# Kernel optimization log

Hardware: AMD Instinct MI355X
Metric: run time of the kernel (lower is better)

The kernel has to match this reference:

```python
import jax, jax.numpy as jnp
import numpy as np

ALPHA = 1.702
LIMIT = 7.0
BLOCK = 32  # mxfp4 block size (values per scale)

# fp4 e2m1 lookup table, indexed by 4-bit code (sign in high bit)
FP4_LUT = jnp.array([0.0, 0.5, 1.0, 1.5, 2.0, 3.0, 4.0, 6.0,
                     -0.0, -0.5, -1.0, -1.5, -2.0, -3.0, -4.0, -6.0],
                    dtype=jnp.float32)


def dequant_mxfp4(blocks, scales):
    # blocks: [E, R, C//2] int byte values (two fp4 nibbles per byte, low nibble first)
    # scales: [E, R, C//32] e8m0 exponents; value = 2^(scale - 127)
    E, R, _ = blocks.shape
    nb = scales.shape[-1]
    lo = blocks & 0xF
    hi = (blocks >> 4) & 0xF
    vals = jnp.stack([FP4_LUT[lo], FP4_LUT[hi]], axis=-1)  # [E,R,C//2,2]
    vals = vals.reshape(E, R, nb, BLOCK)
    scale = jnp.exp2((scales - 127).astype(jnp.float32))   # [E,R,nb]
    return (vals * scale[..., None]).reshape(E, R, nb * BLOCK)  # [E,R,C]


def setup_inputs() -> dict:
    key = jax.random.key(0)
    ks = jax.random.split(key, 12)
    T, E, H, I = 1024, 8, 1024, 1024
    inp = {
        'hidden_states': jax.random.normal(ks[0], (T, H), dtype=jnp.float32),
        'router_logits': jax.random.normal(ks[1], (T, E), dtype=jnp.float32),
        'gate_proj_blocks': jax.random.randint(ks[2], (E, I, H // 2), 0, 256, dtype=jnp.int32),
        'gate_proj_scales': jax.random.randint(ks[3], (E, I, H // BLOCK), 121, 130, dtype=jnp.int32),
        'gate_proj_bias': jax.random.normal(ks[4], (E, I), dtype=jnp.float32) * 0.02,
        'up_proj_blocks': jax.random.randint(ks[5], (E, I, H // 2), 0, 256, dtype=jnp.int32),
        'up_proj_scales': jax.random.randint(ks[6], (E, I, H // BLOCK), 121, 130, dtype=jnp.int32),
        'up_proj_bias': jax.random.normal(ks[7], (E, I), dtype=jnp.float32) * 0.02,
        'down_proj_blocks': jax.random.randint(ks[8], (E, H, I // 2), 0, 256, dtype=jnp.int32),
        'down_proj_scales': jax.random.randint(ks[9], (E, H, I // BLOCK), 121, 130, dtype=jnp.int32),
        'down_proj_bias': jax.random.normal(ks[10], (E, H), dtype=jnp.float32) * 0.02,
        'k': 2,
    }
    return inp


def reference(hidden_states, router_logits, gate_proj_blocks, gate_proj_scales,
              gate_proj_bias, up_proj_blocks, up_proj_scales, up_proj_bias,
              down_proj_blocks, down_proj_scales, down_proj_bias, k):
    T, H = hidden_states.shape
    E = router_logits.shape[-1]
    # --- top-k routing: softmax over the selected logits, scattered to [T,E] ---
    top_vals, top_idx = jax.lax.top_k(router_logits, k)        # [T,k]
    top_w = jax.nn.softmax(top_vals, axis=-1)                   # [T,k]
    route = jnp.zeros((T, E), dtype=hidden_states.dtype)
    route = route.at[jnp.arange(T)[:, None], top_idx].add(top_w)  # [T,E]
    # --- dequantize mxfp4 expert weights ---
    gate_w = dequant_mxfp4(gate_proj_blocks, gate_proj_scales)  # [E,I,H]
    up_w = dequant_mxfp4(up_proj_blocks, up_proj_scales)        # [E,I,H]
    down_w = dequant_mxfp4(down_proj_blocks, down_proj_scales)  # [E,H,I]
    # --- GLU expert FFN (GPT-OSS variant) ---
    gate = jnp.einsum('th,eih->tei', hidden_states, gate_w) + gate_proj_bias[None]
    up = jnp.einsum('th,eih->tei', hidden_states, up_w) + up_proj_bias[None]
    gate = jnp.minimum(gate, LIMIT)
    up = jnp.clip(up, -LIMIT, LIMIT)
    glu = gate * jax.nn.sigmoid(gate * ALPHA)
    act = (up + 1.0) * glu                                       # [T,E,I]
    # fold routing weight in before the down projection, then sum over experts
    act = act * route[:, :, None]
    out = jnp.einsum('tei,ehi->th', act, down_w) + route @ down_proj_bias  # [T,H]
    return out
```

## Files before the change

kernel.cpp:

```cpp
#include <hip/hip_runtime.h>
#include <cstdint>
#include <cstddef>

typedef __bf16 bf16x8 __attribute__((ext_vector_type(8)));
typedef __bf16 bf16x2 __attribute__((ext_vector_type(2)));
typedef float f32x4 __attribute__((ext_vector_type(4)));
typedef unsigned short u16x2 __attribute__((ext_vector_type(2)));

constexpr int HH = 1024;
constexpr int II = 1024;
constexpr int KMAX = 2;
constexpr int EMAX = 8;
constexpr int GU_TILES = 24;
constexpr int DN_TILES = 40;
constexpr float FALPHA = 1.702f;
constexpr float FLIMIT = 7.0f;

#if __has_builtin(__builtin_amdgcn_cvt_scalef32_pk_bf16_fp4)
#define USE_CVT 1
#else
#define USE_CVT 0
#endif

#define SCHED0() __builtin_amdgcn_sched_barrier(0)

__device__ __forceinline__ unsigned pk_add16(unsigned a, unsigned b) {
  u16x2 x, y;
  __builtin_memcpy(&x, &a, 4); __builtin_memcpy(&y, &b, 4);
  u16x2 r = x + y;
  unsigned o; __builtin_memcpy(&o, &r, 4); return o;
}
__device__ __forceinline__ int4 decode_chunk(int4 raw, unsigned addk) {
  unsigned p = (unsigned)raw.x | ((unsigned)raw.y << 8) |
               ((unsigned)raw.z << 16) | ((unsigned)raw.w << 24);
  unsigned q = p >> 4;
  unsigned me = p & 0x07070707u, mo = q & 0x07070707u;
  unsigned se = p & 0x08080808u, so = q & 0x08080808u;
  unsigned hiE = __builtin_amdgcn_perm(0x40404040u, 0x3F3F3F14u, me) | (se << 4);
  unsigned hiO = __builtin_amdgcn_perm(0x40404040u, 0x3F3F3F14u, mo) | (so << 4);
  unsigned loE = __builtin_amdgcn_perm(0xC0804000u, 0xC0800000u, me);
  unsigned loO = __builtin_amdgcn_perm(0xC0804000u, 0xC0800000u, mo);
  int4 out;
  out.x = (int)pk_add16(__builtin_amdgcn_perm(hiE, loE, 0x05010400u), addk);
  out.y = (int)pk_add16(__builtin_amdgcn_perm(hiE, loE, 0x07030602u), addk);
  out.z = (int)pk_add16(__builtin_amdgcn_perm(hiO, loO, 0x05010400u), addk);
  out.w = (int)pk_add16(__builtin_amdgcn_perm(hiO, loO, 0x07030602u), addk);
  return out;
}
__device__ __forceinline__ unsigned make_addk(int s) {
  int k = s - 127;
  unsigned t = ((unsigned)(k << 7)) & 0xFFFFu;
  return t | (t << 16);
}

__device__ __forceinline__ bf16x8 decode_frag(int4 raw, int s) {
#if USE_CVT
  unsigned t0 = __builtin_amdgcn_perm((unsigned)raw.y, (unsigned)raw.x, 0x00000400u);
  unsigned t1 = __builtin_amdgcn_perm((unsigned)raw.w, (unsigned)raw.z, 0x00000400u);
  unsigned p  = __builtin_amdgcn_perm(t1, t0, 0x05040100u);
  float scf = __uint_as_float((unsigned)s << 23);
  bf16x2 a = __builtin_amdgcn_cvt_scalef32_pk_bf16_fp4(p, scf, 0);
  bf16x2 b = __builtin_amdgcn_cvt_scalef32_pk_bf16_fp4(p, scf, 1);
  bf16x2 c = __builtin_amdgcn_cvt_scalef32_pk_bf16_fp4(p, scf, 2);
  bf16x2 d = __builtin_amdgcn_cvt_scalef32_pk_bf16_fp4(p, scf, 3);
  bf16x8 r;
  r[0]=a[0]; r[1]=a[1]; r[2]=b[0]; r[3]=b[1]; r[4]=c[0]; r[5]=c[1]; r[6]=d[0]; r[7]=d[1];
  return r;
#else
  int4 d4 = decode_chunk(raw, make_addk(s));
  bf16x8 r; __builtin_memcpy(&r, &d4, 16);
  return r;
#endif
}

__device__ __forceinline__ void gll16(const void* g, void* l) {
  __builtin_amdgcn_global_load_lds(
      (const __attribute__((address_space(1))) void*)g,
      (__attribute__((address_space(3))) void*)l, 16, 0, 0);
}

__global__ void routing_kernel(const float* __restrict__ logits, const int* __restrict__ dk,
                               int T, int E, float* __restrict__ route,
                               int* __restrict__ tidx, float* __restrict__ tw) {
  int t = blockIdx.x * blockDim.x + threadIdx.x;
  if (t >= T) return;
  int kk = *dk; if (kk > KMAX) kk = KMAX; if (kk < 1) kk = 1;
  int EE = E > EMAX ? EMAX : E;
  float v[EMAX]; bool used[EMAX];
  for (int e = 0; e < EE; ++e) { v[e] = logits[t * E + e]; used[e] = false; route[t * E + e] = 0.f; }
  float tv[KMAX]; int ti[KMAX];
  for (int j = 0; j < kk; ++j) {
    float best = -3.4e38f; int bi = 0;
    for (int e = 0; e < EE; ++e) if (!used[e] && v[e] > best) { best = v[e]; bi = e; }
    used[bi] = true; tv[j] = best; ti[j] = bi;
  }
  float mx = tv[0], ssum = 0.f, wj[KMAX];
  for (int j = 0; j < kk; ++j) { wj[j] = __expf(tv[j] - mx); ssum += wj[j]; }
  for (int j = 0; j < kk; ++j) {
    float wv = wj[j] / ssum;
    route[t * E + ti[j]] = wv;
    tidx[t * kk + j] = ti[j];
    tw[t * kk + j] = wv;
  }
}

__global__ void build_lists(const int* __restrict__ tidx, const int* __restrict__ dk,
                            int T, int* __restrict__ lists, int* __restrict__ counts) {
  int e = blockIdx.x;
  int lane = threadIdx.x;
  int kk = *dk; if (kk > KMAX) kk = KMAX; if (kk < 1) kk = 1;
  int cnt = 0;
  for (int base = 0; base < T; base += 64) {
    int t = base + lane;
    int j = -1;
    if (t < T) {
      for (int q = 0; q < kk; ++q) if (tidx[t * kk + q] == e) j = q;
    }
    unsigned long long m = __ballot(j >= 0);
    if (j >= 0) {
      int pre = __popcll(m & ((1ull << lane) - 1ull));
      lists[e * T + cnt + pre] = (t << 3) | j;
    }
    cnt += __popcll(m);
  }
  if (lane == 0) counts[e] = cnt;
}

__global__ void build_tiles(const int* __restrict__ counts, int E,
                            int* __restrict__ tabGU, int* __restrict__ tabDN) {
  if (threadIdx.x == 0 && blockIdx.x == 0) {
    int g = 0, d = 0;
    for (int e = 0; e < E && e < EMAX; ++e) {
      int c = counts[e];
      for (int m = 0; m * 128 < c && g < GU_TILES; ++m) tabGU[g++] = (e << 16) | m;
      for (int m = 0; m * 64 < c && d < DN_TILES; ++m) tabDN[d++] = (e << 16) | m;
    }
    for (; g < GU_TILES; ++g) tabGU[g] = -1;
    for (; d < DN_TILES; ++d) tabDN[d] = -1;
  }
}

__global__ void convert_hs(const float* __restrict__ hs, __bf16* __restrict__ hsb, int n8) {
  int g = blockIdx.x * 256 + threadIdx.x;
  if (g >= n8) return;
  const float4* p = (const float4*)hs + (size_t)g * 2;
  float4 a = p[0], b = p[1];
  bf16x8 r;
#if USE_CVT
  r[0] = (__bf16)a.x; r[1] = (__bf16)a.y; r[2] = (__bf16)a.z; r[3] = (__bf16)a.w;
  r[4] = (__bf16)b.x; r[5] = (__bf16)b.y; r[6] = (__bf16)b.z; r[7] = (__bf16)b.w;
#else
  r[0] = (__bf16)a.x; r[1] = (__bf16)a.z; r[2] = (__bf16)b.x; r[3] = (__bf16)b.z;
  r[4] = (__bf16)a.y; r[5] = (__bf16)a.w; r[6] = (__bf16)b.y; r[7] = (__bf16)b.w;
#endif
  *(bf16x8*)(hsb + (size_t)g * 8) = r;
}

__global__ __launch_bounds__(256, 2) void gemm_gate_up(
    const __bf16* __restrict__ hsb,
    const int* __restrict__ gblk, const int* __restrict__ gscl, const float* __restrict__ gbias,
    const int* __restrict__ ublk, const int* __restrict__ uscl, const float* __restrict__ ubias,
    const int* __restrict__ lists, const int* __restrict__ counts,
    const float* __restrict__ tw, const int* __restrict__ dk,
    const int* __restrict__ tab,
    __bf16* __restrict__ act, int T)
{
  int te = tab[blockIdx.x];
  if (te < 0) return;
  int e = te >> 16, mtile = te & 0xFFFF;
  int cnt = counts[e];
  int n_valid = cnt - mtile * 128;
  if (n_valid <= 0) return;
  if (n_valid > 128) n_valid = 128;
  int kk = *dk; if (kk > KMAX) kk = KMAX; if (kk < 1) kk = 1;

  __shared__ int s_tok[128];
  __shared__ __attribute__((aligned(16))) char Abuf[2][16384];
  __shared__ __attribute__((aligned(16))) char Braw[2][16384];
  __shared__ __attribute__((aligned(8))) unsigned short sScl[2][64][36];

  int tid = threadIdx.x;
  if (tid < 128) {
    int idx = mtile * 128 + tid;
    s_tok[tid] = lists[e * T + (idx < cnt ? idx : mtile * 128)];
  }
  __syncthreads();

  int lane = tid & 63, w = tid >> 6;
  int r15 = lane & 15, kg = lane >> 4;
  int wr = w >> 1, wc = w & 1;
  int cA = (lane & 7) ^ (lane >> 3);
  int ibase = blockIdx.y * 64;

  unsigned aOff[4];
  #pragma unroll
  for (int q = 0; q < 4; ++q) {
    int row = w * 32 + q * 8 + (lane >> 3);
    int tok = s_tok[row] >> 3;
    aOff[q] = (unsigned)tok * (HH * 2) + (unsigned)cA * 16;
  }
  const char* bSrc[4];
  #pragma unroll
  for (int q = 0; q < 4; ++q) {
    int row = w * 32 + q * 8 + (lane >> 3);
    int mat = (row >> 4) & 1;
    int i = ibase + ((row >> 5) << 4) + (row & 15);
    const int* base = mat ? ublk : gblk;
    bSrc[q] = (const char*)(base + ((size_t)e * II + i) * (HH / 2)) + cA * 16;
  }

  #pragma unroll
  for (int q = 0; q < 4; ++q) {
    gll16((const char*)hsb + aOff[q], Abuf[0] + (w * 32 + q * 8) * 128);
    gll16(bSrc[q], Braw[0] + (w * 32 + q * 8) * 128);
  }
  #pragma unroll
  for (int q = 0; q < 4; ++q) {
    gll16((const char*)hsb + aOff[q] + 128, Abuf[1] + (w * 32 + q * 8) * 128);
    gll16(bSrc[q] + 128, Braw[1] + (w * 32 + q * 8) * 128);
  }

  for (int idx = tid; idx < 1024; idx += 256) {
    int sgm = idx >> 9, rem = idx & 511;
    int row = rem >> 3, c4 = rem & 7;
    const int* base = sgm ? uscl : gscl;
    int4 v = *((const int4*)(base + ((size_t)e * II + ibase + row) * 32) + c4);
    unsigned short* dst = &sScl[sgm][row][c4 * 4];
    dst[0] = (unsigned short)v.x; dst[1] = (unsigned short)v.y;
    dst[2] = (unsigned short)v.z; dst[3] = (unsigned short)v.w;
  }
  __syncthreads();

  f32x4 acc[4][4];
  #pragma unroll
  for (int a = 0; a < 4; ++a)
    #pragma unroll
    for (int b = 0; b < 4; ++b) acc[a][b] = (f32x4)0.f;

  constexpr int NK = HH / 64;
  #pragma unroll 1
  for (int t = 0; t < NK; ++t) {
    if (t > 0) {
      if (t < NK - 1) { asm volatile("s_waitcnt vmcnt(8)" ::: "memory"); }
      else            { asm volatile("s_waitcnt vmcnt(0)" ::: "memory"); }
      SCHED0();
      __builtin_amdgcn_s_barrier();
      SCHED0();
    }
    const char* Ac = Abuf[t & 1];
    const char* Bc = Braw[t & 1];
    unsigned sv[4];
    #pragma unroll
    for (int fn = 0; fn < 4; ++fn) {
      int mat = fn & 1;
      int il = (wc * 2 + (fn >> 1)) * 16 + r15;
      sv[fn] = *(const unsigned*)((const char*)sScl + (mat * 64 + il) * 72 + t * 4);
    }
    #pragma unroll
    for (int kq = 0; kq < 2; ++kq) {
      int kc = kq * 4 + kg;
      bf16x8 bfr[4];
      #pragma unroll
      for (int fn = 0; fn < 4; ++fn) {
        int n = wc * 64 + fn * 16 + r15;
        int4 raw = *(const int4*)(Bc + n * 128 + ((kc ^ (n & 7)) << 4));
        int s = kq ? (int)(sv[fn] >> 16) : (int)(sv[fn] & 0xFFFF);
        bfr[fn] = decode_frag(raw, s);
      }
      #pragma unroll
      for (int fm = 0; fm < 4; ++fm) {
        int m = wr * 64 + fm * 16 + r15;
        bf16x8 af = *(const bf16x8*)(Ac + m * 128 + ((kc ^ (m & 7)) << 4));
        #pragma unroll
        for (int fn = 0; fn < 4; ++fn)
          acc[fm][fn] = __builtin_amdgcn_mfma_f32_16x16x32_bf16(af, bfr[fn], acc[fm][fn], 0, 0, 0);
      }
    }
    if (t + 2 < NK) {
      asm volatile("s_waitcnt lgkmcnt(0)" ::: "memory");
      SCHED0();
      __builtin_amdgcn_s_barrier();
      SCHED0();
      char* An = Abuf[t & 1];
      char* Bn = Braw[t & 1];
      #pragma unroll
      for (int q = 0; q < 4; ++q) {
        gll16((const char*)hsb + aOff[q] + (t + 2) * 128, An + (w * 32 + q * 8) * 128);
        gll16(bSrc[q] + (t + 2) * 128, Bn + (w * 32 + q * 8) * 128);
      }
    }
  }

  #pragma unroll
  for (int p = 0; p < 2; ++p) {
    int i_log = ibase + wc * 32 + p * 16 + r15;
    float gb = gbias[e * II + i_log], ub = ubias[e * II + i_log];
#if USE_CVT
    int i_st = i_log;
#else
    int i_st = (i_log & ~7) | ((i_log & 1) << 2) | ((i_log & 7) >> 1);
#endif
    #pragma unroll
    for (int fm = 0; fm < 4; ++fm) {
      #pragma unroll
      for (int rg = 0; rg < 4; ++rg) {
        int mloc = wr * 64 + fm * 16 + kg * 4 + rg;
        if (mloc < n_valid) {
          int entry = s_tok[mloc];
          int t2 = entry >> 3, j = entry & 7;
          float wv = tw[t2 * kk + j];
          float g = fminf(acc[fm][p * 2][rg] + gb, FLIMIT);
          float u = fminf(fmaxf(acc[fm][p * 2 + 1][rg] + ub, -FLIMIT), FLIMIT);
          float glu = g / (1.f + __expf(-FALPHA * g));
          act[((size_t)t2 * kk + j) * II + i_st] = (__bf16)((u + 1.f) * glu * wv);
        }
      }
    }
  }
}

__global__ __launch_bounds__(256, 2) void gemm_down(
    const __bf16* __restrict__ act,
    const int* __restrict__ dblk, const int* __restrict__ dscl,
    const int* __restrict__ lists, const int* __restrict__ counts,
    const int* __restrict__ dk, const int* __restrict__ tab,
    __bf16* __restrict__ partial, int T)
{
  int te = tab[blockIdx.x];
  if (te < 0) return;
  int e = te >> 16, mtile = te & 0xFFFF;
  int cnt = counts[e];
  int n_valid = cnt - mtile * 64;
  if (n_valid <= 0) return;
  if (n_valid > 64) n_valid = 64;
  int kk = *dk; if (kk > KMAX) kk = KMAX; if (kk < 1) kk = 1;

  __shared__ int s_tok[64];
  __shared__ __attribute__((aligned(16))) char Abuf[2][8192];
  __shared__ __attribute__((aligned(16))) char Braw[2][16384];
  __shared__ __attribute__((aligned(8))) unsigned short sScl[128][36];

  int tid = threadIdx.x;
  if (tid < 64) {
    int idx = mtile * 64 + tid;
    s_tok[tid] = lists[e * T + (idx < cnt ? idx : mtile * 64)];
  }
  __syncthreads();

  int lane = tid & 63, w = tid >> 6;
  int r15 = lane & 15, kg = lane >> 4;
  int wr = w >> 1, wc = w & 1;
  int cA = (lane & 7) ^ (lane >> 3);
  int hbase = blockIdx.y * 128;

  unsigned aOff[2];
  #pragma unroll
  for (int q = 0; q < 2; ++q) {
    int row = w * 16 + q * 8 + (lane >> 3);
    int entry = s_tok[row];
    unsigned slot = (unsigned)(entry >> 3) * kk + (entry & 7);
    aOff[q] = slot * (II * 2) + (unsigned)cA * 16;
  }
  const char* bSrc[4];
  #pragma unroll
  for (int q = 0; q < 4; ++q) {
    int row = w * 32 + q * 8 + (lane >> 3);
    int h = hbase + row;
    bSrc[q] = (const char*)(dblk + ((size_t)e * HH + h) * (II / 2)) + cA * 16;
  }

  #pragma unroll
  for (int q = 0; q < 2; ++q)
    gll16((const char*)act + aOff[q], Abuf[0] + (w * 16 + q * 8) * 128);
  #pragma unroll
  for (int q = 0; q < 4; ++q)
    gll16(bSrc[q], Braw[0] + (w * 32 + q * 8) * 128);
  #pragma unroll
  for (int q = 0; q < 2; ++q)
    gll16((const char*)act + aOff[q] + 128, Abuf[1] + (w * 16 + q * 8) * 128);
  #pragma unroll
  for (int q = 0; q < 4; ++q)
    gll16(bSrc[q] + 128, Braw[1] + (w * 32 + q * 8) * 128);

  for (int idx = tid; idx < 1024; idx += 256) {
    int row = idx >> 3, c4 = idx & 7;
    int4 v = *((const int4*)(dscl + ((size_t)e * HH + hbase + row) * 32) + c4);
    unsigned short* dst = &sScl[row][c4 * 4];
    dst[0] = (unsigned short)v.x; dst[1] = (unsigned short)v.y;
    dst[2] = (unsigned short)v.z; dst[3] = (unsigned short)v.w;
  }
  __syncthreads();

  f32x4 acc[2][4];
  #pragma unroll
  for (int a = 0; a < 2; ++a)
    #pragma unroll
    for (int b = 0; b < 4; ++b) acc[a][b] = (f32x4)0.f;

  constexpr int NK = II / 64;
  #pragma unroll 1
  for (int t = 0; t < NK; ++t) {
    if (t > 0) {
      if (t < NK - 1) { asm volatile("s_waitcnt vmcnt(6)" ::: "memory"); }
      else            { asm volatile("s_waitcnt vmcnt(0)" ::: "memory"); }
      SCHED0();
      __builtin_amdgcn_s_barrier();
      SCHED0();
    }
    const char* Ac = Abuf[t & 1];
    const char* Bc = Braw[t & 1];
    unsigned sv[4];
    #pragma unroll
    for (int fn = 0; fn < 4; ++fn) {
      int n = wc * 64 + fn * 16 + r15;
      sv[fn] = *(const unsigned*)((const char*)sScl + n * 72 + t * 4);
    }
    #pragma unroll
    for (int kq = 0; kq < 2; ++kq) {
      int kc = kq * 4 + kg;
      bf16x8 bfr[4];
      #pragma unroll
      for (int fn = 0; fn < 4; ++fn) {
        int n = wc * 64 + fn * 16 + r15;
        int4 raw = *(const int4*)(Bc + n * 128 + ((kc ^ (n & 7)) << 4));
        int s = kq ? (int)(sv[fn] >> 16) : (int)(sv[fn] & 0xFFFF);
        bfr[fn] = decode_frag(raw, s);
      }
      #pragma unroll
      for (int fm = 0; fm < 2; ++fm) {
        int m = wr * 32 + fm * 16 + r15;
        bf16x8 af = *(const bf16x8*)(Ac + m * 128 + ((kc ^ (m & 7)) << 4));
        #pragma unroll
        for (int fn = 0; fn < 4; ++fn)
          acc[fm][fn] = __builtin_amdgcn_mfma_f32_16x16x32_bf16(af, bfr[fn], acc[fm][fn], 0, 0, 0);
      }
    }
    if (t + 2 < NK) {
      asm volatile("s_waitcnt lgkmcnt(0)" ::: "memory");
      SCHED0();
      __builtin_amdgcn_s_barrier();
      SCHED0();
      char* An = Abuf[t & 1];
      char* Bn = Braw[t & 1];
      #pragma unroll
      for (int q = 0; q < 2; ++q)
        gll16((const char*)act + aOff[q] + (t + 2) * 128, An + (w * 16 + q * 8) * 128);
      #pragma unroll
      for (int q = 0; q < 4; ++q)
        gll16(bSrc[q] + (t + 2) * 128, Bn + (w * 32 + q * 8) * 128);
    }
  }

  #pragma unroll
  for (int fm = 0; fm < 2; ++fm) {
    #pragma unroll
    for (int rg = 0; rg < 4; ++rg) {
      int mloc = wr * 32 + fm * 16 + kg * 4 + rg;
      if (mloc < n_valid) {
        int entry = s_tok[mloc];
        int t2 = entry >> 3, j = entry & 7;
        size_t slot = (size_t)t2 * kk + j;
        #pragma unroll
        for (int fn = 0; fn < 4; ++fn) {
          int h = hbase + wc * 64 + fn * 16 + r15;
          partial[slot * HH + h] = (__bf16)acc[fm][fn][rg];
        }
      }
    }
  }
}

__global__ void combine_kernel(const __bf16* __restrict__ partial, const float* __restrict__ route,
                               const float* __restrict__ dbias, const int* __restrict__ dk,
                               float* __restrict__ out, int E) {
  int t = blockIdx.y;
  int h = blockIdx.x * 256 + threadIdx.x;
  int kk = *dk; if (kk > KMAX) kk = KMAX; if (kk < 1) kk = 1;
  float s = 0.f;
  for (int j = 0; j < kk; ++j) s += (float)partial[((size_t)t * kk + j) * HH + h];
  for (int e = 0; e < E; ++e) s += route[t * E + e] * dbias[(size_t)e * HH + h];
  out[(size_t)t * HH + h] = s;
}

extern "C" void kernel_launch(void* const* d_in, const int* in_sizes, int n_in,
                              void* d_out, int out_size, void* d_ws, size_t ws_size,
                              hipStream_t stream) {
  const float* hs    = (const float*)d_in[0];
  const float* rl    = (const float*)d_in[1];
  const int*   gblk  = (const int*)d_in[2];
  const int*   gscl  = (const int*)d_in[3];
  const float* gbias = (const float*)d_in[4];
  const int*   ublk  = (const int*)d_in[5];
  const int*   uscl  = (const int*)d_in[6];
  const float* ubias = (const float*)d_in[7];
  const int*   dblk  = (const int*)d_in[8];
  const int*   dscl  = (const int*)d_in[9];
  const float* dbias = (const float*)d_in[10];
  const int*   dk    = (const int*)d_in[11];

  long s0 = in_sizes[0], s1 = in_sizes[1], s2 = in_sizes[2], s4 = in_sizes[4];
  int H = (int)(2 * s2 / s4);
  int T = (int)(s0 / H);
  int E = (int)(s1 / T);

  char* w = (char*)d_ws;
  auto alloc = [&](size_t bytes) { char* p = w; w += (bytes + 255) & ~size_t(255); return p; };
  float*  route   = (float*)alloc(sizeof(float) * (size_t)T * E);
  int*    tidx    = (int*)  alloc(sizeof(int)   * (size_t)T * KMAX);
  float*  twp     = (float*)alloc(sizeof(float) * (size_t)T * KMAX);
  int*    counts  = (int*)  alloc(sizeof(int)   * (size_t)E);
  int*    lists   = (int*)  alloc(sizeof(int)   * (size_t)E * T);
  int*    tabGU   = (int*)  alloc(sizeof(int)   * GU_TILES);
  int*    tabDN   = (int*)  alloc(sizeof(int)   * DN_TILES);
  __bf16* hsb     = (__bf16*)alloc(sizeof(__bf16) * (size_t)T * HH);
  __bf16* act     = (__bf16*)alloc(sizeof(__bf16) * (size_t)T * KMAX * II);
  __bf16* partial = (__bf16*)alloc(sizeof(__bf16) * (size_t)T * KMAX * HH);

  routing_kernel<<<dim3((T + 255) / 256), 256, 0, stream>>>(rl, dk, T, E, route, tidx, twp);
  build_lists<<<dim3(E), 64, 0, stream>>>(tidx, dk, T, lists, counts);
  build_tiles<<<dim3(1), 64, 0, stream>>>(counts, E, tabGU, tabDN);
  convert_hs<<<dim3((T * HH / 8 + 255) / 256), 256, 0, stream>>>(hs, hsb, T * HH / 8);
  gemm_gate_up<<<dim3(GU_TILES, II / 64), 256, 0, stream>>>(
      hsb, gblk, gscl, gbias, ublk, uscl, ubias, lists, counts, twp, dk, tabGU, act, T);
  gemm_down<<<dim3(DN_TILES, HH / 128), 256, 0, stream>>>(
      act, dblk, dscl, lists, counts, dk, tabDN, partial, T);
  combine_kernel<<<dim3(HH / 256, T), 256, 0, stream>>>(partial, route, dbias, dk, (float*)d_out, E);
}
```

Baseline: 92.61 us.

## Fuse routing prep into one kernel; shrink GEMM tiles with XCD-swizzled 1D grids

Result: slower. 97.24 us (+5.0%).

```diff
diff --git a/kernel.cpp b/kernel.cpp
--- a/kernel.cpp
+++ b/kernel.cpp
@@ -11,7 +11,7 @@
 constexpr int II = 1024;
 constexpr int KMAX = 2;
 constexpr int EMAX = 8;
-constexpr int GU_TILES = 24;
+constexpr int GU_TILES = 40;
 constexpr int DN_TILES = 40;
 constexpr float FALPHA = 1.702f;
 constexpr float FLIMIT = 7.0f;
@@ -79,60 +79,69 @@
       (__attribute__((address_space(3))) void*)l, 16, 0, 0);
 }
 
-__global__ void routing_kernel(const float* __restrict__ logits, const int* __restrict__ dk,
-                               int T, int E, float* __restrict__ route,
-                               int* __restrict__ tidx, float* __restrict__ tw) {
-  int t = blockIdx.x * blockDim.x + threadIdx.x;
-  if (t >= T) return;
+__device__ __forceinline__ int xcd_swz(int wg, int nwg) {
+  int q = nwg >> 3, r = nwg & 7;
+  int xcd = wg & 7, pos = wg >> 3;
+  return (xcd < r ? xcd * (q + 1) : r * (q + 1) + (xcd - r) * q) + pos;
+}
+
+__global__ __launch_bounds__(1024) void prep_kernel(
+    const float* __restrict__ logits, const int* __restrict__ dk, int T, int E,
+    float* __restrict__ route, float* __restrict__ tw,
+    int* __restrict__ lists, int* __restrict__ counts,
+    int* __restrict__ tabGU, int* __restrict__ tabDN) {
+  __shared__ unsigned char s_ti[1024];
+  __shared__ int s_cnt[EMAX];
+  int t = threadIdx.x;
   int kk = *dk; if (kk > KMAX) kk = KMAX; if (kk < 1) kk = 1;
   int EE = E > EMAX ? EMAX : E;
-  float v[EMAX]; bool used[EMAX];
-  for (int e = 0; e < EE; ++e) { v[e] = logits[t * E + e]; used[e] = false; route[t * E + e] = 0.f; }
-  float tv[KMAX]; int ti[KMAX];
-  for (int j = 0; j < kk; ++j) {
-    float best = -3.4e38f; int bi = 0;
-    for (int e = 0; e < EE; ++e) if (!used[e] && v[e] > best) { best = v[e]; bi = e; }
-    used[bi] = true; tv[j] = best; ti[j] = bi;
-  }
-  float mx = tv[0], ssum = 0.f, wj[KMAX];
-  for (int j = 0; j < kk; ++j) { wj[j] = __expf(tv[j] - mx); ssum += wj[j]; }
-  for (int j = 0; j < kk; ++j) {
-    float wv = wj[j] / ssum;
-    route[t * E + ti[j]] = wv;
-    tidx[t * kk + j] = ti[j];
-    tw[t * kk + j] = wv;
-  }
-}
-
-__global__ void build_lists(const int* __restrict__ tidx, const int* __restrict__ dk,
-                            int T, int* __restrict__ lists, int* __restrict__ counts) {
-  int e = blockIdx.x;
-  int lane = threadIdx.x;
-  int kk = *dk; if (kk > KMAX) kk = KMAX; if (kk < 1) kk = 1;
-  int cnt = 0;
-  for (int base = 0; base < T; base += 64) {
-    int t = base + lane;
-    int j = -1;
-    if (t < T) {
-      for (int q = 0; q < kk; ++q) if (tidx[t * kk + q] == e) j = q;
-    }
-    unsigned long long m = __ballot(j >= 0);
-    if (j >= 0) {
-      int pre = __popcll(m & ((1ull << lane) - 1ull));
-      lists[e * T + cnt + pre] = (t << 3) | j;
-    }
-    cnt += __popcll(m);
-  }
-  if (lane == 0) counts[e] = cnt;
-}
-
-__global__ void build_tiles(const int* __restrict__ counts, int E,
-                            int* __restrict__ tabGU, int* __restrict__ tabDN) {
-  if (threadIdx.x == 0 && blockIdx.x == 0) {
+  if (t < T) {
+    float v[EMAX]; bool used[EMAX];
+    for (int e = 0; e < EE; ++e) { v[e] = logits[t * E + e]; used[e] = false; route[t * E + e] = 0.f; }
+    float tv[KMAX]; int ti[KMAX];
+    for (int j = 0; j < kk; ++j) {
+      float best = -3.4e38f; int bi = 0;
+      for (int e = 0; e < EE; ++e) if (!used[e] && v[e] > best) { best = v[e]; bi = e; }
+      used[bi] = true; tv[j] = best; ti[j] = bi;
+    }
+    float mx = tv[0], ssum = 0.f, wj[KMAX];
+    for (int j = 0; j < kk; ++j) { wj[j] = __expf(tv[j] - mx); ssum += wj[j]; }
+    for (int j = 0; j < kk; ++j) {
+      float wv = wj[j] / ssum;
+      route[t * E + ti[j]] = wv;
+      tw[t * kk + j] = wv;
+    }
+    s_ti[t] = (unsigned char)(ti[0] | ((kk > 1 ? ti[1] : 0xF) << 4));
+  } else if (t < 1024) {
+    s_ti[t] = 0xFF;
+  }
+  __syncthreads();
+  int w = t >> 6, lane = t & 63;
+  if (w < EE) {
+    int e = w, cnt = 0;
+    for (int base = 0; base < T; base += 64) {
+      int tt = base + lane;
+      int j = -1;
+      if (tt < T) {
+        int packed = s_ti[tt];
+        if ((packed & 0xF) == e) j = 0;
+        else if ((packed >> 4) == e) j = 1;
+      }
+      unsigned long long m = __ballot(j >= 0);
+      if (j >= 0) {
+        int pre = __popcll(m & ((1ull << lane) - 1ull));
+        lists[e * T + cnt + pre] = (tt << 3) | j;
+      }
+      cnt += __popcll(m);
+    }
+    if (lane == 0) { counts[e] = cnt; s_cnt[e] = cnt; }
+  }
+  __syncthreads();
+  if (t == 0) {
     int g = 0, d = 0;
-    for (int e = 0; e < E && e < EMAX; ++e) {
-      int c = counts[e];
-      for (int m = 0; m * 128 < c && g < GU_TILES; ++m) tabGU[g++] = (e << 16) | m;
+    for (int e = 0; e < EE; ++e) {
+      int c = s_cnt[e];
+      for (int m = 0; m * 64 < c && g < GU_TILES; ++m) tabGU[g++] = (e << 16) | m;
       for (int m = 0; m * 64 < c && d < DN_TILES; ++m) tabDN[d++] = (e << 16) | m;
     }
     for (; g < GU_TILES; ++g) tabGU[g] = -1;
@@ -156,7 +165,7 @@
   *(bf16x8*)(hsb + (size_t)g * 8) = r;
 }
 
-__global__ __launch_bounds__(256, 2) void gemm_gate_up(
+__global__ __launch_bounds__(128, 4) void gemm_gate_up(
     const __bf16* __restrict__ hsb,
     const int* __restrict__ gblk, const int* __restrict__ gscl, const float* __restrict__ gbias,
     const int* __restrict__ ublk, const int* __restrict__ uscl, const float* __restrict__ ubias,
@@ -165,32 +174,33 @@
     const int* __restrict__ tab,
     __bf16* __restrict__ act, int T)
 {
-  int te = tab[blockIdx.x];
+  int lin = xcd_swz(blockIdx.x, GU_TILES * (II / 16));
+  int ntile = lin / GU_TILES, xt = lin % GU_TILES;
+  int te = tab[xt];
   if (te < 0) return;
   int e = te >> 16, mtile = te & 0xFFFF;
   int cnt = counts[e];
-  int n_valid = cnt - mtile * 128;
+  int n_valid = cnt - mtile * 64;
   if (n_valid <= 0) return;
-  if (n_valid > 128) n_valid = 128;
+  if (n_valid > 64) n_valid = 64;
   int kk = *dk; if (kk > KMAX) kk = KMAX; if (kk < 1) kk = 1;
-
-  __shared__ int s_tok[128];
-  __shared__ __attribute__((aligned(16))) char Abuf[2][16384];
-  __shared__ __attribute__((aligned(16))) char Braw[2][16384];
-  __shared__ __attribute__((aligned(8))) unsigned short sScl[2][64][36];
+  int ibase = ntile * 16;
+
+  __shared__ int s_tok[64];
+  __shared__ __attribute__((aligned(16))) char Abuf[2][8192];
+  __shared__ __attribute__((aligned(16))) char Braw[2][4096];
+  __shared__ __attribute__((aligned(8))) unsigned short sS[32][36];
 
   int tid = threadIdx.x;
-  if (tid < 128) {
-    int idx = mtile * 128 + tid;
-    s_tok[tid] = lists[e * T + (idx < cnt ? idx : mtile * 128)];
+  if (tid < 64) {
+    int idx = mtile * 64 + tid;
+    s_tok[tid] = lists[e * T + (idx < cnt ? idx : mtile * 64)];
   }
   __syncthreads();
 
   int lane = tid & 63, w = tid >> 6;
   int r15 = lane & 15, kg = lane >> 4;
-  int wr = w >> 1, wc = w & 1;
-  int cA = (lane & 7) ^ (lane >> 3);
-  int ibase = blockIdx.y * 64;
+  int cA = (lane & 7) ^ ((lane >> 3) & 7);
 
   unsigned aOff[4];
   #pragma unroll
@@ -199,49 +209,50 @@
     int tok = s_tok[row] >> 3;
     aOff[q] = (unsigned)tok * (HH * 2) + (unsigned)cA * 16;
   }
-  const char* bSrc[4];
-  #pragma unroll
-  for (int q = 0; q < 4; ++q) {
-    int row = w * 32 + q * 8 + (lane >> 3);
+  const char* bSrc[2];
+  #pragma unroll
+  for (int q = 0; q < 2; ++q) {
+    int row = w * 16 + q * 8 + (lane >> 3);
     int mat = (row >> 4) & 1;
-    int i = ibase + ((row >> 5) << 4) + (row & 15);
+    int i = ibase + (row & 15);
     const int* base = mat ? ublk : gblk;
     bSrc[q] = (const char*)(base + ((size_t)e * II + i) * (HH / 2)) + cA * 16;
   }
 
   #pragma unroll
-  for (int q = 0; q < 4; ++q) {
+  for (int q = 0; q < 4; ++q)
     gll16((const char*)hsb + aOff[q], Abuf[0] + (w * 32 + q * 8) * 128);
-    gll16(bSrc[q], Braw[0] + (w * 32 + q * 8) * 128);
-  }
-  #pragma unroll
-  for (int q = 0; q < 4; ++q) {
+  #pragma unroll
+  for (int q = 0; q < 2; ++q)
+    gll16(bSrc[q], Braw[0] + (w * 16 + q * 8) * 128);
+  #pragma unroll
+  for (int q = 0; q < 4; ++q)
     gll16((const char*)hsb + aOff[q] + 128, Abuf[1] + (w * 32 + q * 8) * 128);
-    gll16(bSrc[q] + 128, Braw[1] + (w * 32 + q * 8) * 128);
-  }
-
-  for (int idx = tid; idx < 1024; idx += 256) {
-    int sgm = idx >> 9, rem = idx & 511;
-    int row = rem >> 3, c4 = rem & 7;
-    const int* base = sgm ? uscl : gscl;
-    int4 v = *((const int4*)(base + ((size_t)e * II + ibase + row) * 32) + c4);
-    unsigned short* dst = &sScl[sgm][row][c4 * 4];
+  #pragma unroll
+  for (int q = 0; q < 2; ++q)
+    gll16(bSrc[q] + 128, Braw[1] + (w * 16 + q * 8) * 128);
+
+  for (int idx = tid; idx < 256; idx += 128) {
+    int row = idx >> 3, c4 = idx & 7;
+    int mat = (row >> 4) & 1;
+    int i = ibase + (row & 15);
+    const int* sbase = mat ? uscl : gscl;
+    int4 v = *((const int4*)(sbase + ((size_t)e * II + i) * 32) + c4);
+    unsigned short* dst = &sS[row][c4 * 4];
     dst[0] = (unsigned short)v.x; dst[1] = (unsigned short)v.y;
     dst[2] = (unsigned short)v.z; dst[3] = (unsigned short)v.w;
   }
   __syncthreads();
 
-  f32x4 acc[4][4];
-  #pragma unroll
-  for (int a = 0; a < 4; ++a)
-    #pragma unroll
-    for (int b = 0; b < 4; ++b) acc[a][b] = (f32x4)0.f;
+  f32x4 acc[2][2];
+  #pragma unroll
+  for (int a = 0; a < 2; ++a) { acc[a][0] = (f32x4)0.f; acc[a][1] = (f32x4)0.f; }
 
   constexpr int NK = HH / 64;
   #pragma unroll 1
   for (int t = 0; t < NK; ++t) {
     if (t > 0) {
-      if (t < NK - 1) { asm volatile("s_waitcnt vmcnt(8)" ::: "memory"); }
+      if (t < NK - 1) { asm volatile("s_waitcnt vmcnt(6)" ::: "memory"); }
       else            { asm volatile("s_waitcnt vmcnt(0)" ::: "memory"); }
       SCHED0();
       __builtin_amdgcn_s_barrier();
@@ -249,31 +260,26 @@
     }
     const char* Ac = Abuf[t & 1];
     const char* Bc = Braw[t & 1];
-    unsigned sv[4];
-    #pragma unroll
-    for (int fn = 0; fn < 4; ++fn) {
-      int mat = fn & 1;
-      int il = (wc * 2 + (fn >> 1)) * 16 + r15;
-      sv[fn] = *(const unsigned*)((const char*)sScl + (mat * 64 + il) * 72 + t * 4);
-    }
+    unsigned sv[2];
+    sv[0] = *(const unsigned*)((const char*)sS + (r15) * 72 + t * 4);
+    sv[1] = *(const unsigned*)((const char*)sS + (16 + r15) * 72 + t * 4);
     #pragma unroll
     for (int kq = 0; kq < 2; ++kq) {
       int kc = kq * 4 + kg;
-      bf16x8 bfr[4];
-      #pragma unroll
-      for (int fn = 0; fn < 4; ++fn) {
-        int n = wc * 64 + fn * 16 + r15;
+      bf16x8 bfr[2];
+      #pragma unroll
+      for (int fn = 0; fn < 2; ++fn) {
+        int n = fn * 16 + r15;
         int4 raw = *(const int4*)(Bc + n * 128 + ((kc ^ (n & 7)) << 4));
         int s = kq ? (int)(sv[fn] >> 16) : (int)(sv[fn] & 0xFFFF);
         bfr[fn] = decode_frag(raw, s);
       }
       #pragma unroll
-      for (int fm = 0; fm < 4; ++fm) {
-        int m = wr * 64 + fm * 16 + r15;
+      for (int fm = 0; fm < 2; ++fm) {
+        int m = w * 32 + fm * 16 + r15;
         bf16x8 af = *(const bf16x8*)(Ac + m * 128 + ((kc ^ (m & 7)) << 4));
-        #pragma unroll
-        for (int fn = 0; fn < 4; ++fn)
-          acc[fm][fn] = __builtin_amdgcn_mfma_f32_16x16x32_bf16(af, bfr[fn], acc[fm][fn], 0, 0, 0);
+        acc[fm][0] = __builtin_amdgcn_mfma_f32_16x16x32_bf16(af, bfr[0], acc[fm][0], 0, 0, 0);
+        acc[fm][1] = __builtin_amdgcn_mfma_f32_16x16x32_bf16(af, bfr[1], acc[fm][1], 0, 0, 0);
       }
     }
     if (t + 2 < NK) {
@@ -284,16 +290,16 @@
       char* An = Abuf[t & 1];
       char* Bn = Braw[t & 1];
       #pragma unroll
-      for (int q = 0; q < 4; ++q) {
+      for (int q = 0; q < 4; ++q)
         gll16((const char*)hsb + aOff[q] + (t + 2) * 128, An + (w * 32 + q * 8) * 128);
-        gll16(bSrc[q] + (t + 2) * 128, Bn + (w * 32 + q * 8) * 128);
-      }
-    }
-  }
-
-  #pragma unroll
-  for (int p = 0; p < 2; ++p) {
-    int i_log = ibase + wc * 32 + p * 16 + r15;
+      #pragma unroll
+      for (int q = 0; q < 2; ++q)
+        gll16(bSrc[q] + (t + 2) * 128, Bn + (w * 16 + q * 8) * 128);
+    }
+  }
+
+  {
+    int i_log = ibase + r15;
     float gb = gbias[e * II + i_log], ub = ubias[e * II + i_log];
 #if USE_CVT
     int i_st = i_log;
@@ -301,16 +307,16 @@
     int i_st = (i_log & ~7) | ((i_log & 1) << 2) | ((i_log & 7) >> 1);
 #endif
     #pragma unroll
-    for (int fm = 0; fm < 4; ++fm) {
+    for (int fm = 0; fm < 2; ++fm) {
       #pragma unroll
       for (int rg = 0; rg < 4; ++rg) {
-        int mloc = wr * 64 + fm * 16 + kg * 4 + rg;
+        int mloc = w * 32 + fm * 16 + kg * 4 + rg;
         if (mloc < n_valid) {
           int entry = s_tok[mloc];
           int t2 = entry >> 3, j = entry & 7;
           float wv = tw[t2 * kk + j];
-          float g = fminf(acc[fm][p * 2][rg] + gb, FLIMIT);
-          float u = fminf(fmaxf(acc[fm][p * 2 + 1][rg] + ub, -FLIMIT), FLIMIT);
+          float g = fminf(acc[fm][0][rg] + gb, FLIMIT);
+          float u = fminf(fmaxf(acc[fm][1][rg] + ub, -FLIMIT), FLIMIT);
           float glu = g / (1.f + __expf(-FALPHA * g));
           act[((size_t)t2 * kk + j) * II + i_st] = (__bf16)((u + 1.f) * glu * wv);
         }
@@ -319,14 +325,16 @@
   }
 }
 
-__global__ __launch_bounds__(256, 2) void gemm_down(
+__global__ __launch_bounds__(128, 4) void gemm_down(
     const __bf16* __restrict__ act,
     const int* __restrict__ dblk, const int* __restrict__ dscl,
     const int* __restrict__ lists, const int* __restrict__ counts,
     const int* __restrict__ dk, const int* __restrict__ tab,
     __bf16* __restrict__ partial, int T)
 {
-  int te = tab[blockIdx.x];
+  int lin = xcd_swz(blockIdx.x, DN_TILES * (HH / 32));
+  int ntile = lin / DN_TILES, xt = lin % DN_TILES;
+  int te = tab[xt];
   if (te < 0) return;
   int e = te >> 16, mtile = te & 0xFFFF;
   int cnt = counts[e];
@@ -334,11 +342,12 @@
   if (n_valid <= 0) return;
   if (n_valid > 64) n_valid = 64;
   int kk = *dk; if (kk > KMAX) kk = KMAX; if (kk < 1) kk = 1;
+  int hbase = ntile * 32;
 
   __shared__ int s_tok[64];
   __shared__ __attribute__((aligned(16))) char Abuf[2][8192];
-  __shared__ __attribute__((aligned(16))) char Braw[2][16384];
-  __shared__ __attribute__((aligned(8))) unsigned short sScl[128][36];
+  __shared__ __attribute__((aligned(16))) char Braw[2][4096];
+  __shared__ __attribute__((aligned(8))) unsigned short sS[32][36];
 
   int tid = threadIdx.x;
   if (tid < 64) {
@@ -349,53 +358,48 @@
 
   int lane = tid & 63, w = tid >> 6;
   int r15 = lane & 15, kg = lane >> 4;
-  int wr = w >> 1, wc = w & 1;
-  int cA = (lane & 7) ^ (lane >> 3);
-  int hbase = blockIdx.y * 128;
-
-  unsigned aOff[2];
-  #pragma unroll
-  for (int q = 0; q < 2; ++q) {
-    int row = w * 16 + q * 8 + (lane >> 3);
+  int cA = (lane & 7) ^ ((lane >> 3) & 7);
+
+  unsigned aOff[4];
+  #pragma unroll
+  for (int q = 0; q < 4; ++q) {
+    int row = w * 32 + q * 8 + (lane >> 3);
     int entry = s_tok[row];
     unsigned slot = (unsigned)(entry >> 3) * kk + (entry & 7);
     aOff[q] = slot * (II * 2) + (unsigned)cA * 16;
   }
-  const char* bSrc[4];
-  #pragma unroll
-  for (int q = 0; q < 4; ++q) {
-    int row = w * 32 + q * 8 + (lane >> 3);
-    int h = hbase + row;
-    bSrc[q] = (const char*)(dblk + ((size_t)e * HH + h) * (II / 2)) + cA * 16;
-  }
-
+  const char* bSrc[2];
+  #pragma unroll
+  for (int q = 0; q < 2; ++q) {
+    int row = w * 16 + q * 8 + (lane >> 3);
+    bSrc[q] = (const char*)(dblk + ((size_t)e * HH + hbase + row) * (II / 2)) + cA * 16;
+  }
+
+  #pragma unroll
+  for (int q = 0; q < 4; ++q)
+    gll16((const char*)act + aOff[q], Abuf[0] + (w * 32 + q * 8) * 128);
   #pragma unroll
   for (int q = 0; q < 2; ++q)
-    gll16((const char*)act + aOff[q], Abuf[0] + (w * 16 + q * 8) * 128);
+    gll16(bSrc[q], Braw[0] + (w * 16 + q * 8) * 128);
   #pragma unroll
   for (int q = 0; q < 4; ++q)
-    gll16(bSrc[q], Braw[0] + (w * 32 + q * 8) * 128);
+    gll16((const char*)act + aOff[q] + 128, Abuf[1] + (w * 32 + q * 8) * 128);
   #pragma unroll
   for (int q = 0; q < 2; ++q)
-    gll16((const char*)act + aOff[q] + 128, Abuf[1] + (w * 16 + q * 8) * 128);
-  #pragma unroll
-  for (int q = 0; q < 4; ++q)
-    gll16(bSrc[q] + 128, Braw[1] + (w * 32 + q * 8) * 128);
-
-  for (int idx = tid; idx < 1024; idx += 256) {
+    gll16(bSrc[q] + 128, Braw[1] + (w * 16 + q * 8) * 128);
+
+  for (int idx = tid; idx < 256; idx += 128) {
     int row = idx >> 3, c4 = idx & 7;
     int4 v = *((const int4*)(dscl + ((size_t)e * HH + hbase + row) * 32) + c4);
-    unsigned short* dst = &sScl[row][c4 * 4];
+    unsigned short* dst = &sS[row][c4 * 4];
     dst[0] = (unsigned short)v.x; dst[1] = (unsigned short)v.y;
     dst[2] = (unsigned short)v.z; dst[3] = (unsigned short)v.w;
   }
   __syncthreads();
 
-  f32x4 acc[2][4];
-  #pragma unroll
-  for (int a = 0; a < 2; ++a)
-    #pragma unroll
-    for (int b = 0; b < 4; ++b) acc[a][b] = (f32x4)0.f;
+  f32x4 acc[2][2];
+  #pragma unroll
+  for (int a = 0; a < 2; ++a) { acc[a][0] = (f32x4)0.f; acc[a][1] = (f32x4)0.f; }
 
   constexpr int NK = II / 64;
   #pragma unroll 1
@@ -409,30 +413,26 @@
     }
     const char* Ac = Abuf[t & 1];
     const char* Bc = Braw[t & 1];
-    unsigned sv[4];
-    #pragma unroll
-    for (int fn = 0; fn < 4; ++fn) {
-      int n = wc * 64 + fn * 16 + r15;
-      sv[fn] = *(const unsigned*)((const char*)sScl + n * 72 + t * 4);
-    }
+    unsigned sv[2];
+    sv[0] = *(const unsigned*)((const char*)sS + (r15) * 72 + t * 4);
+    sv[1] = *(const unsigned*)((const char*)sS + (16 + r15) * 72 + t * 4);
     #pragma unroll
     for (int kq = 0; kq < 2; ++kq) {
       int kc = kq * 4 + kg;
-      bf16x8 bfr[4];
-      #pragma unroll
-      for (int fn = 0; fn < 4; ++fn) {
-        int n = wc * 64 + fn * 16 + r15;
+      bf16x8 bfr[2];
+      #pragma unroll
+      for (int fn = 0; fn < 2; ++fn) {
+        int n = fn * 16 + r15;
         int4 raw = *(const int4*)(Bc + n * 128 + ((kc ^ (n & 7)) << 4));
         int s = kq ? (int)(sv[fn] >> 16) : (int)(sv[fn] & 0xFFFF);
         bfr[fn] = decode_frag(raw, s);
       }
       #pragma unroll
       for (int fm = 0; fm < 2; ++fm) {
-        int m = wr * 32 + fm * 16 + r15;
+        int m = w * 32 + fm * 16 + r15;
         bf16x8 af = *(const bf16x8*)(Ac + m * 128 + ((kc ^ (m & 7)) << 4));
-        #pragma unroll
-        for (int fn = 0; fn < 4; ++fn)
-          acc[fm][fn] = __builtin_amdgcn_mfma_f32_16x16x32_bf16(af, bfr[fn], acc[fm][fn], 0, 0, 0);
+        acc[fm][0] = __builtin_amdgcn_mfma_f32_16x16x32_bf16(af, bfr[0], acc[fm][0], 0, 0, 0);
+        acc[fm][1] = __builtin_amdgcn_mfma_f32_16x16x32_bf16(af, bfr[1], acc[fm][1], 0, 0, 0);
       }
     }
     if (t + 2 < NK) {
@@ -443,11 +443,11 @@
       char* An = Abuf[t & 1];
       char* Bn = Braw[t & 1];
       #pragma unroll
+      for (int q = 0; q < 4; ++q)
+        gll16((const char*)act + aOff[q] + (t + 2) * 128, An + (w * 32 + q * 8) * 128);
+      #pragma unroll
       for (int q = 0; q < 2; ++q)
-        gll16((const char*)act + aOff[q] + (t + 2) * 128, An + (w * 16 + q * 8) * 128);
-      #pragma unroll
-      for (int q = 0; q < 4; ++q)
-        gll16(bSrc[q] + (t + 2) * 128, Bn + (w * 32 + q * 8) * 128);
+        gll16(bSrc[q] + (t + 2) * 128, Bn + (w * 16 + q * 8) * 128);
     }
   }
 
@@ -455,14 +455,14 @@
   for (int fm = 0; fm < 2; ++fm) {
     #pragma unroll
     for (int rg = 0; rg < 4; ++rg) {
-      int mloc = wr * 32 + fm * 16 + kg * 4 + rg;
+      int mloc = w * 32 + fm * 16 + kg * 4 + rg;
       if (mloc < n_valid) {
         int entry = s_tok[mloc];
         int t2 = entry >> 3, j = entry & 7;
         size_t slot = (size_t)t2 * kk + j;
         #pragma unroll
-        for (int fn = 0; fn < 4; ++fn) {
-          int h = hbase + wc * 64 + fn * 16 + r15;
+        for (int fn = 0; fn < 2; ++fn) {
+          int h = hbase + fn * 16 + r15;
           partial[slot * HH + h] = (__bf16)acc[fm][fn][rg];
         }
       }
@@ -506,7 +506,6 @@
   char* w = (char*)d_ws;
   auto alloc = [&](size_t bytes) { char* p = w; w += (bytes + 255) & ~size_t(255); return p; };
   float*  route   = (float*)alloc(sizeof(float) * (size_t)T * E);
-  int*    tidx    = (int*)  alloc(sizeof(int)   * (size_t)T * KMAX);
   float*  twp     = (float*)alloc(sizeof(float) * (size_t)T * KMAX);
   int*    counts  = (int*)  alloc(sizeof(int)   * (size_t)E);
   int*    lists   = (int*)  alloc(sizeof(int)   * (size_t)E * T);
@@ -516,13 +515,11 @@
   __bf16* act     = (__bf16*)alloc(sizeof(__bf16) * (size_t)T * KMAX * II);
   __bf16* partial = (__bf16*)alloc(sizeof(__bf16) * (size_t)T * KMAX * HH);
 
-  routing_kernel<<<dim3((T + 255) / 256), 256, 0, stream>>>(rl, dk, T, E, route, tidx, twp);
-  build_lists<<<dim3(E), 64, 0, stream>>>(tidx, dk, T, lists, counts);
-  build_tiles<<<dim3(1), 64, 0, stream>>>(counts, E, tabGU, tabDN);
+  prep_kernel<<<dim3(1), 1024, 0, stream>>>(rl, dk, T, E, route, twp, lists, counts, tabGU, tabDN);
   convert_hs<<<dim3((T * HH / 8 + 255) / 256), 256, 0, stream>>>(hs, hsb, T * HH / 8);
-  gemm_gate_up<<<dim3(GU_TILES, II / 64), 256, 0, stream>>>(
+  gemm_gate_up<<<dim3(GU_TILES * (II / 16)), 128, 0, stream>>>(
       hsb, gblk, gscl, gbias, ublk, uscl, ubias, lists, counts, twp, dk, tabGU, act, T);
-  gemm_down<<<dim3(DN_TILES, HH / 128), 256, 0, stream>>>(
+  gemm_down<<<dim3(DN_TILES * (HH / 32)), 128, 0, stream>>>(
       act, dblk, dscl, lists, counts, dk, tabDN, partial, T);
   combine_kernel<<<dim3(HH / 256, T), 256, 0, stream>>>(partial, route, dbias, dk, (float*)d_out, E);
 }
```
